# Kernel tuning notes

Measured on AMD Instinct MI355X. Metric: run time of the kernel, lower is better.

Reference implementation:

```python
import jax, jax.numpy as jnp
import numpy as np

EMBED_DIM = 512
LQ, LA, T, B = 32, 16, 32, 8192
BN_EPS = 1e-5


def _masked_mean(x, lens):
    # x: [L, B, D] seq-first; lens: [B] int. Mean over the first lens[b] steps.
    L = x.shape[0]
    mask = (jnp.arange(L)[:, None] < lens[None, :]).astype(x.dtype)  # [L, B]
    s = jnp.einsum('lb,lbd->bd', mask, x)
    return s / lens.astype(x.dtype)[:, None]


def setup_inputs() -> dict:
    key = jax.random.key(0)
    ks = jax.random.split(key, 12)
    D = EMBED_DIM
    inp = {
        'question_embedding_v': jax.random.normal(ks[0], (LQ, B, D), jnp.float32),
        'visual_embedding_qu': jax.random.normal(ks[1], (T, B, D), jnp.float32),
        'question_len': jax.random.randint(ks[2], (B,), 1, LQ + 1),
        'answer_embedding_v_expand': jax.random.normal(ks[3], (LA, B, D), jnp.float32),
        'visual_embedding_an_expand': jax.random.normal(ks[4], (T, B, D), jnp.float32),
        'answers_len': jax.random.randint(ks[5], (B,), 1, LA + 1),
    }
    # Classifier params (xavier-normal linears, zero bias; BN gamma=1, beta=0)
    def xavier(k, fan_out, fan_in):
        std = (2.0 / (fan_in + fan_out)) ** 0.5
        return std * jax.random.normal(k, (fan_out, fan_in), jnp.float32)
    inp['W1'] = xavier(ks[6], D, 4 * D)
    inp['b1'] = jnp.zeros((D,), jnp.float32)
    inp['gamma'] = jnp.ones((D,), jnp.float32)
    inp['beta'] = jnp.zeros((D,), jnp.float32)
    inp['W2'] = xavier(ks[7], 1, D)
    inp['b2'] = jnp.zeros((1,), jnp.float32)
    return inp


def reference(question_embedding_v, visual_embedding_qu, question_len,
              answer_embedding_v_expand, visual_embedding_an_expand, answers_len,
              W1, b1, gamma, beta, W2, b2):
    q = _masked_mean(question_embedding_v, question_len)            # [B, D]
    vq = jnp.mean(visual_embedding_qu, axis=0)                      # [B, D]
    a = _masked_mean(answer_embedding_v_expand, answers_len)        # [B, D]
    va = jnp.mean(visual_embedding_an_expand, axis=0)               # [B, D]
    out = jnp.concatenate([q, vq, a, va], axis=1)                   # [B, 4D]
    # Dropout treated as identity (eval / deterministic baseline).
    h = out @ W1.T + b1                                             # [B, D]
    h = jax.nn.gelu(h, approximate=False)                           # torch nn.GELU (exact erf)
    # BatchNorm1d in training mode: biased batch statistics over B.
    mu = jnp.mean(h, axis=0)
    var = jnp.mean(jnp.square(h - mu), axis=0)
    h = (h - mu) * jax.lax.rsqrt(var + BN_EPS) * gamma + beta
    logits = h @ W2.T + b2                                          # [B, 1]
    return logits
```

## Files before the change

kernel.cpp:

```cpp
#include <hip/hip_runtime.h>
#include <hip/hip_bf16.h>
#include <math.h>

typedef unsigned short u16;
typedef unsigned int   u32;
typedef short  short8 __attribute__((ext_vector_type(8)));
typedef float  f32x4  __attribute__((ext_vector_type(4)));

#define EMB 512
#define BB  8192
#define KDIM 2048

__device__ inline u16 f2b(float f) {
    union { float f; u32 u; } v; v.f = f;
    u32 r = v.u + 0x7fffu + ((v.u >> 16) & 1u);
    return (u16)(r >> 16);
}

__global__ __launch_bounds__(256) void k_w1(const float4* __restrict__ w, u16* __restrict__ o) {
    int i = blockIdx.x * 256 + threadIdx.x;
    float4 v = w[i];
    u32 lo = (u32)f2b(v.x) | ((u32)f2b(v.y) << 16);
    u32 hi = (u32)f2b(v.z) | ((u32)f2b(v.w) << 16);
    *(uint2*)(o + (size_t)i * 4) = make_uint2(lo, hi);
}

__global__ __launch_bounds__(128) void k_pool(
    const float* __restrict__ qv, const float* __restrict__ vqu, const int* __restrict__ qlen,
    const float* __restrict__ av, const float* __restrict__ van, const int* __restrict__ alen,
    u16* __restrict__ pooled)
{
    const int b = blockIdx.x;
    const int t = threadIdx.x;
    const size_t rowf = (size_t)BB * EMB;
    const size_t base = (size_t)b * EMB + (size_t)t * 4;
    u16* dst = pooled + (size_t)b * KDIM;

    float4 acc;
    {
        int n = qlen[b];
        acc.x = acc.y = acc.z = acc.w = 0.f;
        const float* p = qv + base;
        for (int l = 0; l < n; ++l) {
            float4 v = *(const float4*)(p + (size_t)l * rowf);
            acc.x += v.x; acc.y += v.y; acc.z += v.z; acc.w += v.w;
        }
        float inv = 1.0f / (float)n;
        u32 lo = (u32)f2b(acc.x * inv) | ((u32)f2b(acc.y * inv) << 16);
        u32 hi = (u32)f2b(acc.z * inv) | ((u32)f2b(acc.w * inv) << 16);
        *(uint2*)(dst + t * 4) = make_uint2(lo, hi);
    }
    {
        acc.x = acc.y = acc.z = acc.w = 0.f;
        const float* p = vqu + base;
        #pragma unroll 8
        for (int l = 0; l < 32; ++l) {
            float4 v = *(const float4*)(p + (size_t)l * rowf);
            acc.x += v.x; acc.y += v.y; acc.z += v.z; acc.w += v.w;
        }
        const float inv = 1.0f / 32.0f;
        u32 lo = (u32)f2b(acc.x * inv) | ((u32)f2b(acc.y * inv) << 16);
        u32 hi = (u32)f2b(acc.z * inv) | ((u32)f2b(acc.w * inv) << 16);
        *(uint2*)(dst + EMB + t * 4) = make_uint2(lo, hi);
    }
    {
        int n = alen[b];
        acc.x = acc.y = acc.z = acc.w = 0.f;
        const float* p = av + base;
        for (int l = 0; l < n; ++l) {
            float4 v = *(const float4*)(p + (size_t)l * rowf);
            acc.x += v.x; acc.y += v.y; acc.z += v.z; acc.w += v.w;
        }
        float inv = 1.0f / (float)n;
        u32 lo = (u32)f2b(acc.x * inv) | ((u32)f2b(acc.y * inv) << 16);
        u32 hi = (u32)f2b(acc.z * inv) | ((u32)f2b(acc.w * inv) << 16);
        *(uint2*)(dst + 2 * EMB + t * 4) = make_uint2(lo, hi);
    }
    {
        acc.x = acc.y = acc.z = acc.w = 0.f;
        const float* p = van + base;
        #pragma unroll 8
        for (int l = 0; l < 32; ++l) {
            float4 v = *(const float4*)(p + (size_t)l * rowf);
            acc.x += v.x; acc.y += v.y; acc.z += v.z; acc.w += v.w;
        }
        const float inv = 1.0f / 32.0f;
        u32 lo = (u32)f2b(acc.x * inv) | ((u32)f2b(acc.y * inv) << 16);
        u32 hi = (u32)f2b(acc.z * inv) | ((u32)f2b(acc.w * inv) << 16);
        *(uint2*)(dst + 3 * EMB + t * 4) = make_uint2(lo, hi);
    }
}

#define GBM 64
#define GBN 128
#define GBK 64
__global__ __launch_bounds__(256) void k_gemm(
    const u16* __restrict__ A, const u16* __restrict__ Bw,
    const float* __restrict__ bias, float* __restrict__ H)
{
    __shared__ u16 As[GBM * GBK];
    __shared__ u16 Bs[GBN * GBK];

    const int tid  = threadIdx.x;
    const int lane = tid & 63;
    const int wid  = tid >> 6;
    const int brow = blockIdx.y * GBM;
    const int bcol = blockIdx.x * GBN;

    const int lrow = lane & 15;
    const int lko  = (lane >> 4) * 8;

    f32x4 acc[4][2];
    #pragma unroll
    for (int m = 0; m < 4; ++m)
        #pragma unroll
        for (int n = 0; n < 2; ++n)
            acc[m][n] = (f32x4){0.f, 0.f, 0.f, 0.f};

    for (int kt = 0; kt < KDIM / GBK; ++kt) {
        const int k0 = kt * GBK;
        #pragma unroll
        for (int i = 0; i < 2; ++i) {
            int flat = i * 256 + tid;
            int row  = flat >> 3;
            int c8   = (flat & 7) * 8;
            const u16* src = A + (size_t)(brow + row) * KDIM + k0 + c8;
            u16* dst = &As[flat * 8];
            __builtin_amdgcn_global_load_lds(
                (const __attribute__((address_space(1))) void*)src,
                (__attribute__((address_space(3))) void*)dst, 16, 0, 0);
        }
        #pragma unroll
        for (int i = 0; i < 4; ++i) {
            int flat = i * 256 + tid;
            int row  = flat >> 3;
            int c8   = (flat & 7) * 8;
            const u16* src = Bw + (size_t)(bcol + row) * KDIM + k0 + c8;
            u16* dst = &Bs[flat * 8];
            __builtin_amdgcn_global_load_lds(
                (const __attribute__((address_space(1))) void*)src,
                (__attribute__((address_space(3))) void*)dst, 16, 0, 0);
        }
        __syncthreads();
        #pragma unroll
        for (int kk = 0; kk < 2; ++kk) {
            short8 bfrag[2];
            #pragma unroll
            for (int n = 0; n < 2; ++n)
                bfrag[n] = *(const short8*)&Bs[(wid * 32 + n * 16 + lrow) * GBK + kk * 32 + lko];
            #pragma unroll
            for (int m = 0; m < 4; ++m) {
                short8 afrag = *(const short8*)&As[(m * 16 + lrow) * GBK + kk * 32 + lko];
                #pragma unroll
                for (int n = 0; n < 2; ++n)
                    acc[m][n] = __builtin_amdgcn_mfma_f32_16x16x32_bf16(
                        afrag, bfrag[n], acc[m][n], 0, 0, 0);
            }
        }
        __syncthreads();
    }

    #pragma unroll
    for (int m = 0; m < 4; ++m) {
        const int row0 = brow + m * 16 + (lane >> 4) * 4;
        #pragma unroll
        for (int n = 0; n < 2; ++n) {
            const int col = bcol + wid * 32 + n * 16 + (lane & 15);
            const float bv = bias[col];
            #pragma unroll
            for (int r = 0; r < 4; ++r) {
                float x = acc[m][n][r] + bv;
                float g = 0.5f * x * (1.0f + erff(x * 0.70710678118654752f));
                H[(size_t)(row0 + r) * EMB + col] = g;
            }
        }
    }
}

__global__ __launch_bounds__(512) void k_stats(const float* __restrict__ H,
                                               float* __restrict__ psum,
                                               float* __restrict__ psq)
{
    const int f = threadIdx.x;
    const int j = blockIdx.x;
    const float* p = H + (size_t)j * 128 * EMB + f;
    float s = 0.f, ss = 0.f;
    #pragma unroll 4
    for (int r = 0; r < 128; ++r) {
        float v = p[(size_t)r * EMB];
        s += v; ss += v * v;
    }
    psum[j * EMB + f] = s;
    psq [j * EMB + f] = ss;
}

__global__ __launch_bounds__(512) void k_fin(const float* __restrict__ psum,
                                             const float* __restrict__ psq,
                                             const float* __restrict__ gamma,
                                             const float* __restrict__ beta,
                                             const float* __restrict__ W2,
                                             const float* __restrict__ b2,
                                             float* __restrict__ coeff)
{
    const int f = threadIdx.x;
    float s = 0.f, ss = 0.f;
    for (int j = 0; j < 64; ++j) { s += psum[j * EMB + f]; ss += psq[j * EMB + f]; }
    const float invB = 1.0f / 8192.0f;
    float mu  = s * invB;
    float var = ss * invB - mu * mu;
    float rs  = rsqrtf(var + 1e-5f);
    float c   = gamma[f] * rs * W2[f];
    coeff[f]  = c;
    float kterm = beta[f] * W2[f] - mu * c;

    __shared__ float red[512];
    red[f] = kterm;
    __syncthreads();
    for (int s2 = 256; s2 > 0; s2 >>= 1) {
        if (f < s2) red[f] += red[f + s2];
        __syncthreads();
    }
    if (f == 0) coeff[512] = red[0] + b2[0];
}

__global__ __launch_bounds__(64) void k_logits(const float* __restrict__ H,
                                               const float* __restrict__ coeff,
                                               float* __restrict__ out)
{
    const int b = blockIdx.x;
    const int l = threadIdx.x;
    const float4* hp = (const float4*)(H + (size_t)b * EMB);
    const float4* cp = (const float4*)coeff;
    float4 h0 = hp[l],      c0 = cp[l];
    float4 h1 = hp[l + 64], c1 = cp[l + 64];
    float p = h0.x * c0.x + h0.y * c0.y + h0.z * c0.z + h0.w * c0.w
            + h1.x * c1.x + h1.y * c1.y + h1.z * c1.z + h1.w * c1.w;
    #pragma unroll
    for (int off = 32; off > 0; off >>= 1) p += __shfl_down(p, off);
    if (l == 0) out[b] = p + coeff[512];
}

extern "C" void kernel_launch(void* const* d_in, const int* in_sizes, int n_in,
                              void* d_out, int out_size, void* d_ws, size_t ws_size,
                              hipStream_t stream) {
    (void)in_sizes; (void)n_in; (void)out_size; (void)ws_size;
    const float* qv    = (const float*)d_in[0];
    const float* vqu   = (const float*)d_in[1];
    const int*   qlen  = (const int*)d_in[2];
    const float* av    = (const float*)d_in[3];
    const float* van   = (const float*)d_in[4];
    const int*   alen  = (const int*)d_in[5];
    const float* W1    = (const float*)d_in[6];
    const float* b1    = (const float*)d_in[7];
    const float* gamma = (const float*)d_in[8];
    const float* beta  = (const float*)d_in[9];
    const float* W2    = (const float*)d_in[10];
    const float* b2    = (const float*)d_in[11];
    float* out = (float*)d_out;

    char* ws = (char*)d_ws;
    u16*   pooled = (u16*)(ws);
    u16*   w1b    = (u16*)(ws + 33554432);
    float* H      = (float*)(ws + 35651584);
    float* psum   = (float*)(ws + 52428800);
    float* psq    = (float*)(ws + 52559872);
    float* coeff  = (float*)(ws + 52690944);

    k_w1    <<<dim3(1024),   dim3(256), 0, stream>>>((const float4*)W1, w1b);
    k_pool  <<<dim3(8192),   dim3(128), 0, stream>>>(qv, vqu, qlen, av, van, alen, pooled);
    k_gemm  <<<dim3(4, 128), dim3(256), 0, stream>>>(pooled, w1b, b1, H);
    k_stats <<<dim3(64),     dim3(512), 0, stream>>>(H, psum, psq);
    k_fin   <<<dim3(1),      dim3(512), 0, stream>>>(psum, psq, gamma, beta, W2, b2, coeff);
    k_logits<<<dim3(8192),   dim3(64),  0, stream>>>(H, coeff, out);
}
```

Baseline: 381.6 us.

## Restructure pooling: two batch rows per wave, nontemporal loads, widen stats grid

The pooling kernel now assigns two batch rows to each 64-lane wave. Each lane keeps four float4 accumulators, and the input streams through nontemporal vector loads with wave-uniform sequence lengths taken via readfirstlane. The goal is more loads in flight per thread and less cache pollution from the read-once activation stream, which dominates runtime. Separately, the BN statistics kernel is split into 256 blocks of 32 rows instead of 64 blocks of 128 rows for better parallelism, which gives the final reduction more partials to sum.

Result: faster. 351.5 us (-7.9%).

```diff
diff --git a/kernel.cpp b/kernel.cpp
--- a/kernel.cpp
+++ b/kernel.cpp
@@ -15,6 +15,10 @@
     union { float f; u32 u; } v; v.f = f;
     u32 r = v.u + 0x7fffu + ((v.u >> 16) & 1u);
     return (u16)(r >> 16);
+}
+
+__device__ inline f32x4 ntload(const float* p) {
+    return __builtin_nontemporal_load((const f32x4*)p);
 }
 
 __global__ __launch_bounds__(256) void k_w1(const float4* __restrict__ w, u16* __restrict__ o) {
@@ -25,69 +29,131 @@
     *(uint2*)(o + (size_t)i * 4) = make_uint2(lo, hi);
 }
 
-__global__ __launch_bounds__(128) void k_pool(
+__global__ __launch_bounds__(256) void k_pool(
     const float* __restrict__ qv, const float* __restrict__ vqu, const int* __restrict__ qlen,
     const float* __restrict__ av, const float* __restrict__ van, const int* __restrict__ alen,
     u16* __restrict__ pooled)
 {
-    const int b = blockIdx.x;
-    const int t = threadIdx.x;
+    const int tid  = threadIdx.x;
+    const int w    = tid >> 6;
+    const int lane = tid & 63;
+    const int bA   = blockIdx.x * 8 + 2 * w;
     const size_t rowf = (size_t)BB * EMB;
-    const size_t base = (size_t)b * EMB + (size_t)t * 4;
-    u16* dst = pooled + (size_t)b * KDIM;
-
-    float4 acc;
+
+    u16* dstA = pooled + (size_t)bA * KDIM;
+    u16* dstB = pooled + (size_t)(bA + 1) * KDIM;
+
     {
-        int n = qlen[b];
-        acc.x = acc.y = acc.z = acc.w = 0.f;
-        const float* p = qv + base;
-        for (int l = 0; l < n; ++l) {
-            float4 v = *(const float4*)(p + (size_t)l * rowf);
-            acc.x += v.x; acc.y += v.y; acc.z += v.z; acc.w += v.w;
-        }
-        float inv = 1.0f / (float)n;
-        u32 lo = (u32)f2b(acc.x * inv) | ((u32)f2b(acc.y * inv) << 16);
-        u32 hi = (u32)f2b(acc.z * inv) | ((u32)f2b(acc.w * inv) << 16);
-        *(uint2*)(dst + t * 4) = make_uint2(lo, hi);
+        const int nA = __builtin_amdgcn_readfirstlane(qlen[bA]);
+        const int nB = __builtin_amdgcn_readfirstlane(qlen[bA + 1]);
+        const int mx = nA > nB ? nA : nB;
+        f32x4 a0 = {0,0,0,0}, a1 = a0, a2 = a0, a3 = a0;
+        const float* p = qv + (size_t)bA * EMB + lane * 4;
+        #pragma unroll 2
+        for (int l = 0; l < mx; ++l) {
+            const float* r = p + (size_t)l * rowf;
+            if (l < nA) {
+                f32x4 v0 = ntload(r), v1 = ntload(r + 256);
+                a0 += v0; a1 += v1;
+            }
+            if (l < nB) {
+                f32x4 v2 = ntload(r + 512), v3 = ntload(r + 768);
+                a2 += v2; a3 += v3;
+            }
+        }
+        const float iA = 1.0f / (float)nA, iB = 1.0f / (float)nB;
+        *(uint2*)(dstA + lane * 4) =
+            make_uint2((u32)f2b(a0.x*iA) | ((u32)f2b(a0.y*iA) << 16),
+                       (u32)f2b(a0.z*iA) | ((u32)f2b(a0.w*iA) << 16));
+        *(uint2*)(dstA + (lane + 64) * 4) =
+            make_uint2((u32)f2b(a1.x*iA) | ((u32)f2b(a1.y*iA) << 16),
+                       (u32)f2b(a1.z*iA) | ((u32)f2b(a1.w*iA) << 16));
+        *(uint2*)(dstB + lane * 4) =
+            make_uint2((u32)f2b(a2.x*iB) | ((u32)f2b(a2.y*iB) << 16),
+                       (u32)f2b(a2.z*iB) | ((u32)f2b(a2.w*iB) << 16));
+        *(uint2*)(dstB + (lane + 64) * 4) =
+            make_uint2((u32)f2b(a3.x*iB) | ((u32)f2b(a3.y*iB) << 16),
+                       (u32)f2b(a3.z*iB) | ((u32)f2b(a3.w*iB) << 16));
     }
     {
-        acc.x = acc.y = acc.z = acc.w = 0.f;
-        const float* p = vqu + base;
-        #pragma unroll 8
+        f32x4 a0 = {0,0,0,0}, a1 = a0, a2 = a0, a3 = a0;
+        const float* p = vqu + (size_t)bA * EMB + lane * 4;
+        #pragma unroll 4
         for (int l = 0; l < 32; ++l) {
-            float4 v = *(const float4*)(p + (size_t)l * rowf);
-            acc.x += v.x; acc.y += v.y; acc.z += v.z; acc.w += v.w;
-        }
-        const float inv = 1.0f / 32.0f;
-        u32 lo = (u32)f2b(acc.x * inv) | ((u32)f2b(acc.y * inv) << 16);
-        u32 hi = (u32)f2b(acc.z * inv) | ((u32)f2b(acc.w * inv) << 16);
-        *(uint2*)(dst + EMB + t * 4) = make_uint2(lo, hi);
+            const float* r = p + (size_t)l * rowf;
+            f32x4 v0 = ntload(r),       v1 = ntload(r + 256);
+            f32x4 v2 = ntload(r + 512), v3 = ntload(r + 768);
+            a0 += v0; a1 += v1; a2 += v2; a3 += v3;
+        }
+        const float iv = 1.0f / 32.0f;
+        *(uint2*)(dstA + EMB + lane * 4) =
+            make_uint2((u32)f2b(a0.x*iv) | ((u32)f2b(a0.y*iv) << 16),
+                       (u32)f2b(a0.z*iv) | ((u32)f2b(a0.w*iv) << 16));
+        *(uint2*)(dstA + EMB + (lane + 64) * 4) =
+            make_uint2((u32)f2b(a1.x*iv) | ((u32)f2b(a1.y*iv) << 16),
+                       (u32)f2b(a1.z*iv) | ((u32)f2b(a1.w*iv) << 16));
+        *(uint2*)(dstB + EMB + lane * 4) =
+            make_uint2((u32)f2b(a2.x*iv) | ((u32)f2b(a2.y*iv) << 16),
+                       (u32)f2b(a2.z*iv) | ((u32)f2b(a2.w*iv) << 16));
+        *(uint2*)(dstB + EMB + (lane + 64) * 4) =
+            make_uint2((u32)f2b(a3.x*iv) | ((u32)f2b(a3.y*iv) << 16),
+                       (u32)f2b(a3.z*iv) | ((u32)f2b(a3.w*iv) << 16));
     }
     {
-        int n = alen[b];
-        acc.x = acc.y = acc.z = acc.w = 0.f;
-        const float* p = av + base;
-        for (int l = 0; l < n; ++l) {
-            float4 v = *(const float4*)(p + (size_t)l * rowf);
-            acc.x += v.x; acc.y += v.y; acc.z += v.z; acc.w += v.w;
-        }
-        float inv = 1.0f / (float)n;
-        u32 lo = (u32)f2b(acc.x * inv) | ((u32)f2b(acc.y * inv) << 16);
-        u32 hi = (u32)f2b(acc.z * inv) | ((u32)f2b(acc.w * inv) << 16);
-        *(uint2*)(dst + 2 * EMB + t * 4) = make_uint2(lo, hi);
+        const int nA = __builtin_amdgcn_readfirstlane(alen[bA]);
+        const int nB = __builtin_amdgcn_readfirstlane(alen[bA + 1]);
+        const int mx = nA > nB ? nA : nB;
+        f32x4 a0 = {0,0,0,0}, a1 = a0, a2 = a0, a3 = a0;
+        const float* p = av + (size_t)bA * EMB + lane * 4;
+        #pragma unroll 2
+        for (int l = 0; l < mx; ++l) {
+            const float* r = p + (size_t)l * rowf;
+            if (l < nA) {
+                f32x4 v0 = ntload(r), v1 = ntload(r + 256);
+                a0 += v0; a1 += v1;
+            }
+            if (l < nB) {
+                f32x4 v2 = ntload(r + 512), v3 = ntload(r + 768);
+                a2 += v2; a3 += v3;
+            }
+        }
+        const float iA = 1.0f / (float)nA, iB = 1.0f / (float)nB;
+        *(uint2*)(dstA + 2 * EMB + lane * 4) =
+            make_uint2((u32)f2b(a0.x*iA) | ((u32)f2b(a0.y*iA) << 16),
+                       (u32)f2b(a0.z*iA) | ((u32)f2b(a0.w*iA) << 16));
+        *(uint2*)(dstA + 2 * EMB + (lane + 64) * 4) =
+            make_uint2((u32)f2b(a1.x*iA) | ((u32)f2b(a1.y*iA) << 16),
+                       (u32)f2b(a1.z*iA) | ((u32)f2b(a1.w*iA) << 16));
+        *(uint2*)(dstB + 2 * EMB + lane * 4) =
+            make_uint2((u32)f2b(a2.x*iB) | ((u32)f2b(a2.y*iB) << 16),
+                       (u32)f2b(a2.z*iB) | ((u32)f2b(a2.w*iB) << 16));
+        *(uint2*)(dstB + 2 * EMB + (lane + 64) * 4) =
+            make_uint2((u32)f2b(a3.x*iB) | ((u32)f2b(a3.y*iB) << 16),
+                       (u32)f2b(a3.z*iB) | ((u32)f2b(a3.w*iB) << 16));
     }
     {
-        acc.x = acc.y = acc.z = acc.w = 0.f;
-        const float* p = van + base;
-        #pragma unroll 8
+        f32x4 a0 = {0,0,0,0}, a1 = a0, a2 = a0, a3 = a0;
+        const float* p = van + (size_t)bA * EMB + lane * 4;
+        #pragma unroll 4
         for (int l = 0; l < 32; ++l) {
-            float4 v = *(const float4*)(p + (size_t)l * rowf);
-            acc.x += v.x; acc.y += v.y; acc.z += v.z; acc.w += v.w;
-        }
-        const float inv = 1.0f / 32.0f;
-        u32 lo = (u32)f2b(acc.x * inv) | ((u32)f2b(acc.y * inv) << 16);
-        u32 hi = (u32)f2b(acc.z * inv) | ((u32)f2b(acc.w * inv) << 16);
-        *(uint2*)(dst + 3 * EMB + t * 4) = make_uint2(lo, hi);
+            const float* r = p + (size_t)l * rowf;
+            f32x4 v0 = ntload(r),       v1 = ntload(r + 256);
+            f32x4 v2 = ntload(r + 512), v3 = ntload(r + 768);
+            a0 += v0; a1 += v1; a2 += v2; a3 += v3;
+        }
+        const float iv = 1.0f / 32.0f;
+        *(uint2*)(dstA + 3 * EMB + lane * 4) =
+            make_uint2((u32)f2b(a0.x*iv) | ((u32)f2b(a0.y*iv) << 16),
+                       (u32)f2b(a0.z*iv) | ((u32)f2b(a0.w*iv) << 16));
+        *(uint2*)(dstA + 3 * EMB + (lane + 64) * 4) =
+            make_uint2((u32)f2b(a1.x*iv) | ((u32)f2b(a1.y*iv) << 16),
+                       (u32)f2b(a1.z*iv) | ((u32)f2b(a1.w*iv) << 16));
+        *(uint2*)(dstB + 3 * EMB + lane * 4) =
+            make_uint2((u32)f2b(a2.x*iv) | ((u32)f2b(a2.y*iv) << 16),
+                       (u32)f2b(a2.z*iv) | ((u32)f2b(a2.w*iv) << 16));
+        *(uint2*)(dstB + 3 * EMB + (lane + 64) * 4) =
+            make_uint2((u32)f2b(a3.x*iv) | ((u32)f2b(a3.y*iv) << 16),
+                       (u32)f2b(a3.z*iv) | ((u32)f2b(a3.w*iv) << 16));
     }
 }
 
@@ -183,10 +249,10 @@
 {
     const int f = threadIdx.x;
     const int j = blockIdx.x;
-    const float* p = H + (size_t)j * 128 * EMB + f;
+    const float* p = H + (size_t)j * 32 * EMB + f;
     float s = 0.f, ss = 0.f;
     #pragma unroll 4
-    for (int r = 0; r < 128; ++r) {
+    for (int r = 0; r < 32; ++r) {
         float v = p[(size_t)r * EMB];
         s += v; ss += v * v;
     }
@@ -204,7 +270,7 @@
 {
     const int f = threadIdx.x;
     float s = 0.f, ss = 0.f;
-    for (int j = 0; j < 64; ++j) { s += psum[j * EMB + f]; ss += psq[j * EMB + f]; }
+    for (int j = 0; j < 256; ++j) { s += psum[j * EMB + f]; ss += psq[j * EMB + f]; }
     const float invB = 1.0f / 8192.0f;
     float mu  = s * invB;
     float var = ss * invB - mu * mu;
@@ -263,13 +329,13 @@
     u16*   w1b    = (u16*)(ws + 33554432);
     float* H      = (float*)(ws + 35651584);
     float* psum   = (float*)(ws + 52428800);
-    float* psq    = (float*)(ws + 52559872);
-    float* coeff  = (float*)(ws + 52690944);
+    float* psq    = (float*)(ws + 52953088);
+    float* coeff  = (float*)(ws + 53477376);
 
     k_w1    <<<dim3(1024),   dim3(256), 0, stream>>>((const float4*)W1, w1b);
-    k_pool  <<<dim3(8192),   dim3(128), 0, stream>>>(qv, vqu, qlen, av, van, alen, pooled);
+    k_pool  <<<dim3(1024),   dim3(256), 0, stream>>>(qv, vqu, qlen, av, van, alen, pooled);
     k_gemm  <<<dim3(4, 128), dim3(256), 0, stream>>>(pooled, w1b, b1, H);
-    k_stats <<<dim3(64),     dim3(512), 0, stream>>>(H, psum, psq);
+    k_stats <<<dim3(256),    dim3(512), 0, stream>>>(H, psum, psq);
     k_fin   <<<dim3(1),      dim3(512), 0, stream>>>(psum, psq, gamma, beta, W2, b2, coeff);
     k_logits<<<dim3(8192),   dim3(64),  0, stream>>>(H, coeff, out);
 }
```

## Split pooling into full and masked mean kernels with nontemporal wide loads

Applied to the files above, without the earlier changes.

Replaces the one-block-per-batch pooling kernel with two kernels. One averages the unmasked visual sequences using 16 independent nontemporal float4 loads per thread per step. The other averages the masked sequences over four batch rows per wave, with the lengths made wave-uniform through readfirstlane. Both aim to raise memory-level parallelism on the bandwidth-bound read of roughly 460MB of activations. The batch-norm statistics kernel is also spread across 256 blocks instead of 64, so k_fin now reduces more partials.

Result: faster. 345.7 us (-9.4%).

```diff
diff --git a/kernel.cpp b/kernel.cpp
--- a/kernel.cpp
+++ b/kernel.cpp
@@ -15,6 +15,10 @@
     union { float f; u32 u; } v; v.f = f;
     u32 r = v.u + 0x7fffu + ((v.u >> 16) & 1u);
     return (u16)(r >> 16);
+}
+
+__device__ inline f32x4 ntload(const float* p) {
+    return __builtin_nontemporal_load((const f32x4*)p);
 }
 
 __global__ __launch_bounds__(256) void k_w1(const float4* __restrict__ w, u16* __restrict__ o) {
@@ -25,69 +29,135 @@
     *(uint2*)(o + (size_t)i * 4) = make_uint2(lo, hi);
 }
 
-__global__ __launch_bounds__(128) void k_pool(
-    const float* __restrict__ qv, const float* __restrict__ vqu, const int* __restrict__ qlen,
-    const float* __restrict__ av, const float* __restrict__ van, const int* __restrict__ alen,
+__global__ __launch_bounds__(256) void k_meanfull(const float* __restrict__ vqu,
+                                                  const float* __restrict__ van,
+                                                  u16* __restrict__ pooled)
+{
+    const int tid = threadIdx.x;
+    const int ln  = tid & 63;
+    int bid = blockIdx.x;
+    const float* src; int sec;
+    if (bid < 256) { src = vqu; sec = 1; }
+    else           { src = van; sec = 3; bid -= 256; }
+    const int g = bid * 4 + (tid >> 6);
+    const size_t rowf = (size_t)BB * EMB;
+
+    f32x4 acc[16];
+    #pragma unroll
+    for (int j = 0; j < 16; ++j) acc[j] = (f32x4){0.f, 0.f, 0.f, 0.f};
+
+    const float* p0 = src + (size_t)g * 4096 + ln * 4;
+    for (int l = 0; l < 32; ++l) {
+        const float* p = p0 + (size_t)l * rowf;
+        f32x4 v[16];
+        #pragma unroll
+        for (int j = 0; j < 16; ++j) v[j] = ntload(p + j * 256);
+        #pragma unroll
+        for (int j = 0; j < 16; ++j) acc[j] += v[j];
+    }
+
+    const int bA = g * 8;
+    const float iv = 1.0f / 32.0f;
+    #pragma unroll
+    for (int j = 0; j < 16; ++j) {
+        f32x4 a = acc[j];
+        u16* dst = pooled + (size_t)(bA + (j >> 1)) * KDIM + sec * EMB
+                 + (j & 1) * 256 + ln * 4;
+        *(uint2*)dst = make_uint2((u32)f2b(a.x*iv) | ((u32)f2b(a.y*iv) << 16),
+                                  (u32)f2b(a.z*iv) | ((u32)f2b(a.w*iv) << 16));
+    }
+}
+
+__global__ __launch_bounds__(256) void k_meanmask(
+    const float* __restrict__ qv, const int* __restrict__ qlen,
+    const float* __restrict__ av, const int* __restrict__ alen,
     u16* __restrict__ pooled)
 {
-    const int b = blockIdx.x;
-    const int t = threadIdx.x;
+    const int tid  = threadIdx.x;
+    const int w    = tid >> 6;
+    const int lane = tid & 63;
+    const int bA   = blockIdx.x * 16 + w * 4;
     const size_t rowf = (size_t)BB * EMB;
-    const size_t base = (size_t)b * EMB + (size_t)t * 4;
-    u16* dst = pooled + (size_t)b * KDIM;
-
-    float4 acc;
+
     {
-        int n = qlen[b];
-        acc.x = acc.y = acc.z = acc.w = 0.f;
-        const float* p = qv + base;
-        for (int l = 0; l < n; ++l) {
-            float4 v = *(const float4*)(p + (size_t)l * rowf);
-            acc.x += v.x; acc.y += v.y; acc.z += v.z; acc.w += v.w;
-        }
-        float inv = 1.0f / (float)n;
-        u32 lo = (u32)f2b(acc.x * inv) | ((u32)f2b(acc.y * inv) << 16);
-        u32 hi = (u32)f2b(acc.z * inv) | ((u32)f2b(acc.w * inv) << 16);
-        *(uint2*)(dst + t * 4) = make_uint2(lo, hi);
+        const int n0 = __builtin_amdgcn_readfirstlane(qlen[bA]);
+        const int n1 = __builtin_amdgcn_readfirstlane(qlen[bA + 1]);
+        const int n2 = __builtin_amdgcn_readfirstlane(qlen[bA + 2]);
+        const int n3 = __builtin_amdgcn_readfirstlane(qlen[bA + 3]);
+        int mx = n0 > n1 ? n0 : n1;
+        mx = mx > n2 ? mx : n2; mx = mx > n3 ? mx : n3;
+        f32x4 a0 = {0,0,0,0}, b0 = a0, a1 = a0, b1 = a0,
+              a2 = a0, b2 = a0, a3 = a0, b3 = a0;
+        const float* p = qv + (size_t)bA * EMB + lane * 4;
+        for (int l = 0; l < mx; ++l) {
+            const float* r = p + (size_t)l * rowf;
+            if (l < n0) { f32x4 v = ntload(r),        u = ntload(r + 256);  a0 += v; b0 += u; }
+            if (l < n1) { f32x4 v = ntload(r + 512),  u = ntload(r + 768);  a1 += v; b1 += u; }
+            if (l < n2) { f32x4 v = ntload(r + 1024), u = ntload(r + 1280); a2 += v; b2 += u; }
+            if (l < n3) { f32x4 v = ntload(r + 1536), u = ntload(r + 1792); a3 += v; b3 += u; }
+        }
+        const float i0 = 1.0f/(float)n0, i1 = 1.0f/(float)n1,
+                    i2 = 1.0f/(float)n2, i3 = 1.0f/(float)n3;
+        u16* d0 = pooled + (size_t)(bA    ) * KDIM + lane * 4;
+        u16* d1 = pooled + (size_t)(bA + 1) * KDIM + lane * 4;
+        u16* d2 = pooled + (size_t)(bA + 2) * KDIM + lane * 4;
+        u16* d3 = pooled + (size_t)(bA + 3) * KDIM + lane * 4;
+        *(uint2*)(d0      ) = make_uint2((u32)f2b(a0.x*i0) | ((u32)f2b(a0.y*i0) << 16),
+                                         (u32)f2b(a0.z*i0) | ((u32)f2b(a0.w*i0) << 16));
+        *(uint2*)(d0 + 256) = make_uint2((u32)f2b(b0.x*i0) | ((u32)f2b(b0.y*i0) << 16),
+                                         (u32)f2b(b0.z*i0) | ((u32)f2b(b0.w*i0) << 16));
+        *(uint2*)(d1      ) = make_uint2((u32)f2b(a1.x*i1) | ((u32)f2b(a1.y*i1) << 16),
+                                         (u32)f2b(a1.z*i1) | ((u32)f2b(a1.w*i1) << 16));
+        *(uint2*)(d1 + 256) = make_uint2((u32)f2b(b1.x*i1) | ((u32)f2b(b1.y*i1) << 16),
+                                         (u32)f2b(b1.z*i1) | ((u32)f2b(b1.w*i1) << 16));
+        *(uint2*)(d2      ) = make_uint2((u32)f2b(a2.x*i2) | ((u32)f2b(a2.y*i2) << 16),
+                                         (u32)f2b(a2.z*i2) | ((u32)f2b(a2.w*i2) << 16));
+        *(uint2*)(d2 + 256) = make_uint2((u32)f2b(b2.x*i2) | ((u32)f2b(b2.y*i2) << 16),
+                                         (u32)f2b(b2.z*i2) | ((u32)f2b(b2.w*i2) << 16));
+        *(uint2*)(d3      ) = make_uint2((u32)f2b(a3.x*i3) | ((u32)f2b(a3.y*i3) << 16),
+                                         (u32)f2b(a3.z*i3) | ((u32)f2b(a3.w*i3) << 16));
+        *(uint2*)(d3 + 256) = make_uint2((u32)f2b(b3.x*i3) | ((u32)f2b(b3.y*i3) << 16),
+                                         (u32)f2b(b3.z*i3) | ((u32)f2b(b3.w*i3) << 16));
     }
     {
-        acc.x = acc.y = acc.z = acc.w = 0.f;
-        const float* p = vqu + base;
-        #pragma unroll 8
-        for (int l = 0; l < 32; ++l) {
-            float4 v = *(const float4*)(p + (size_t)l * rowf);
-            acc.x += v.x; acc.y += v.y; acc.z += v.z; acc.w += v.w;
-        }
-        const float inv = 1.0f / 32.0f;
-        u32 lo = (u32)f2b(acc.x * inv) | ((u32)f2b(acc.y * inv) << 16);
-        u32 hi = (u32)f2b(acc.z * inv) | ((u32)f2b(acc.w * inv) << 16);
-        *(uint2*)(dst + EMB + t * 4) = make_uint2(lo, hi);
-    }
-    {
-        int n = alen[b];
-        acc.x = acc.y = acc.z = acc.w = 0.f;
-        const float* p = av + base;
-        for (int l = 0; l < n; ++l) {
-            float4 v = *(const float4*)(p + (size_t)l * rowf);
-            acc.x += v.x; acc.y += v.y; acc.z += v.z; acc.w += v.w;
-        }
-        float inv = 1.0f / (float)n;
-        u32 lo = (u32)f2b(acc.x * inv) | ((u32)f2b(acc.y * inv) << 16);
-        u32 hi = (u32)f2b(acc.z * inv) | ((u32)f2b(acc.w * inv) << 16);
-        *(uint2*)(dst + 2 * EMB + t * 4) = make_uint2(lo, hi);
-    }
-    {
-        acc.x = acc.y = acc.z = acc.w = 0.f;
-        const float* p = van + base;
-        #pragma unroll 8
-        for (int l = 0; l < 32; ++l) {
-            float4 v = *(const float4*)(p + (size_t)l * rowf);
-            acc.x += v.x; acc.y += v.y; acc.z += v.z; acc.w += v.w;
-        }
-        const float inv = 1.0f / 32.0f;
-        u32 lo = (u32)f2b(acc.x * inv) | ((u32)f2b(acc.y * inv) << 16);
-        u32 hi = (u32)f2b(acc.z * inv) | ((u32)f2b(acc.w * inv) << 16);
-        *(uint2*)(dst + 3 * EMB + t * 4) = make_uint2(lo, hi);
+        const int n0 = __builtin_amdgcn_readfirstlane(alen[bA]);
+        const int n1 = __builtin_amdgcn_readfirstlane(alen[bA + 1]);
+        const int n2 = __builtin_amdgcn_readfirstlane(alen[bA + 2]);
+        const int n3 = __builtin_amdgcn_readfirstlane(alen[bA + 3]);
+        int mx = n0 > n1 ? n0 : n1;
+        mx = mx > n2 ? mx : n2; mx = mx > n3 ? mx : n3;
+        f32x4 a0 = {0,0,0,0}, b0 = a0, a1 = a0, b1 = a0,
+              a2 = a0, b2 = a0, a3 = a0, b3 = a0;
+        const float* p = av + (size_t)bA * EMB + lane * 4;
+        for (int l = 0; l < mx; ++l) {
+            const float* r = p + (size_t)l * rowf;
+            if (l < n0) { f32x4 v = ntload(r),        u = ntload(r + 256);  a0 += v; b0 += u; }
+            if (l < n1) { f32x4 v = ntload(r + 512),  u = ntload(r + 768);  a1 += v; b1 += u; }
+            if (l < n2) { f32x4 v = ntload(r + 1024), u = ntload(r + 1280); a2 += v; b2 += u; }
+            if (l < n3) { f32x4 v = ntload(r + 1536), u = ntload(r + 1792); a3 += v; b3 += u; }
+        }
+        const float i0 = 1.0f/(float)n0, i1 = 1.0f/(float)n1,
+                    i2 = 1.0f/(float)n2, i3 = 1.0f/(float)n3;
+        u16* d0 = pooled + (size_t)(bA    ) * KDIM + 2 * EMB + lane * 4;
+        u16* d1 = pooled + (size_t)(bA + 1) * KDIM + 2 * EMB + lane * 4;
+        u16* d2 = pooled + (size_t)(bA + 2) * KDIM + 2 * EMB + lane * 4;
+        u16* d3 = pooled + (size_t)(bA + 3) * KDIM + 2 * EMB + lane * 4;
+        *(uint2*)(d0      ) = make_uint2((u32)f2b(a0.x*i0) | ((u32)f2b(a0.y*i0) << 16),
+                                         (u32)f2b(a0.z*i0) | ((u32)f2b(a0.w*i0) << 16));
+        *(uint2*)(d0 + 256) = make_uint2((u32)f2b(b0.x*i0) | ((u32)f2b(b0.y*i0) << 16),
+                                         (u32)f2b(b0.z*i0) | ((u32)f2b(b0.w*i0) << 16));
+        *(uint2*)(d1      ) = make_uint2((u32)f2b(a1.x*i1) | ((u32)f2b(a1.y*i1) << 16),
+                                         (u32)f2b(a1.z*i1) | ((u32)f2b(a1.w*i1) << 16));
+        *(uint2*)(d1 + 256) = make_uint2((u32)f2b(b1.x*i1) | ((u32)f2b(b1.y*i1) << 16),
+                                         (u32)f2b(b1.z*i1) | ((u32)f2b(b1.w*i1) << 16));
+        *(uint2*)(d2      ) = make_uint2((u32)f2b(a2.x*i2) | ((u32)f2b(a2.y*i2) << 16),
+                                         (u32)f2b(a2.z*i2) | ((u32)f2b(a2.w*i2) << 16));
+        *(uint2*)(d2 + 256) = make_uint2((u32)f2b(b2.x*i2) | ((u32)f2b(b2.y*i2) << 16),
+                                         (u32)f2b(b2.z*i2) | ((u32)f2b(b2.w*i2) << 16));
+        *(uint2*)(d3      ) = make_uint2((u32)f2b(a3.x*i3) | ((u32)f2b(a3.y*i3) << 16),
+                                         (u32)f2b(a3.z*i3) | ((u32)f2b(a3.w*i3) << 16));
+        *(uint2*)(d3 + 256) = make_uint2((u32)f2b(b3.x*i3) | ((u32)f2b(b3.y*i3) << 16),
+                                         (u32)f2b(b3.z*i3) | ((u32)f2b(b3.w*i3) << 16));
     }
 }
 
@@ -183,10 +253,10 @@
 {
     const int f = threadIdx.x;
     const int j = blockIdx.x;
-    const float* p = H + (size_t)j * 128 * EMB + f;
+    const float* p = H + (size_t)j * 32 * EMB + f;
     float s = 0.f, ss = 0.f;
     #pragma unroll 4
-    for (int r = 0; r < 128; ++r) {
+    for (int r = 0; r < 32; ++r) {
         float v = p[(size_t)r * EMB];
         s += v; ss += v * v;
     }
@@ -204,7 +274,7 @@
 {
     const int f = threadIdx.x;
     float s = 0.f, ss = 0.f;
-    for (int j = 0; j < 64; ++j) { s += psum[j * EMB + f]; ss += psq[j * EMB + f]; }
+    for (int j = 0; j < 256; ++j) { s += psum[j * EMB + f]; ss += psq[j * EMB + f]; }
     const float invB = 1.0f / 8192.0f;
     float mu  = s * invB;
     float var = ss * invB - mu * mu;
@@ -263,13 +333,14 @@
     u16*   w1b    = (u16*)(ws + 33554432);
     float* H      = (float*)(ws + 35651584);
     float* psum   = (float*)(ws + 52428800);
-    float* psq    = (float*)(ws + 52559872);
-    float* coeff  = (float*)(ws + 52690944);
-
-    k_w1    <<<dim3(1024),   dim3(256), 0, stream>>>((const float4*)W1, w1b);
-    k_pool  <<<dim3(8192),   dim3(128), 0, stream>>>(qv, vqu, qlen, av, van, alen, pooled);
-    k_gemm  <<<dim3(4, 128), dim3(256), 0, stream>>>(pooled, w1b, b1, H);
-    k_stats <<<dim3(64),     dim3(512), 0, stream>>>(H, psum, psq);
-    k_fin   <<<dim3(1),      dim3(512), 0, stream>>>(psum, psq, gamma, beta, W2, b2, coeff);
-    k_logits<<<dim3(8192),   dim3(64),  0, stream>>>(H, coeff, out);
-}
+    float* psq    = (float*)(ws + 52953088);
+    float* coeff  = (float*)(ws + 53477376);
+
+    k_w1      <<<dim3(1024),   dim3(256), 0, stream>>>((const float4*)W1, w1b);
+    k_meanfull<<<dim3(512),    dim3(256), 0, stream>>>(vqu, van, pooled);
+    k_meanmask<<<dim3(512),    dim3(256), 0, stream>>>(qv, qlen, av, alen, pooled);
+    k_gemm    <<<dim3(4, 128), dim3(256), 0, stream>>>(pooled, w1b, b1, H);
+    k_stats   <<<dim3(256),    dim3(512), 0, stream>>>(H, psum, psq);
+    k_fin     <<<dim3(1),      dim3(512), 0, stream>>>(psum, psq, gamma, beta, W2, b2, coeff);
+    k_logits  <<<dim3(8192),   dim3(64),  0, stream>>>(H, coeff, out);
+}
```
